# Optimization experiments

Hardware: AMD Instinct MI355X
Metric: run time of the kernel (lower is better)

The kernel has to match this reference:

```python
import jax, jax.numpy as jnp
import numpy as np

B, N, C = 2, 1024, 512
H = 8
HD = C // H  # 64
SCALE = HD ** -0.5


def setup_inputs() -> dict:
    key = jax.random.key(0)
    ks = jax.random.split(key, 10)
    q = jax.random.normal(ks[0], (B, N, C), jnp.float32)
    k = jax.random.normal(ks[1], (B, N, C), jnp.float32)
    v = jax.random.normal(ks[2], (B, N, C), jnp.float32)
    rel_pos_bias = jax.random.normal(ks[3], (B, N, N, HD), jnp.float32)
    # float padding mask: 0 for valid tokens, large negative for padded ones
    key_padding_mask = jnp.where(
        jax.random.uniform(ks[4], (B, N)) > 0.1, 0.0, -1e4
    ).astype(jnp.float32)
    Wq = jax.random.normal(ks[5], (C, C), jnp.float32) * 0.02
    Wk = jax.random.normal(ks[6], (C, C), jnp.float32) * 0.02
    Wv = jax.random.normal(ks[7], (C, C), jnp.float32) * 0.02
    Wp = jax.random.normal(ks[8], (C, C), jnp.float32) * 0.02
    bp = jnp.zeros((C,), jnp.float32)
    return {"q": q, "k": k, "v": v, "rel_pos_bias": rel_pos_bias,
            "key_padding_mask": key_padding_mask,
            "Wq": Wq, "Wk": Wk, "Wv": Wv, "Wp": Wp, "bp": bp}


def reference(q, k, v, rel_pos_bias, key_padding_mask, Wq, Wk, Wv, Wp, bp):
    # QKV projections, split heads: [B,H,N,HD]
    qh = (q @ Wq).reshape(B, N, H, HD).transpose(0, 2, 1, 3) * SCALE
    kh = (k @ Wk).reshape(B, N, H, HD).transpose(0, 2, 1, 3)
    vh = (v @ Wv).reshape(B, N, H, HD).transpose(0, 2, 1, 3)
    # scores + relative-bias injection into logits
    attn = jnp.einsum('bhid,bhjd->bhij', qh, kh)
    attn = attn + jnp.einsum('bhic,bijc->bhij', qh, rel_pos_bias)
    # float padding mask -> pairwise additive bias
    m = key_padding_mask
    pair = jnp.minimum(m[:, None, :], m[:, :, None])
    pair = jnp.where(jnp.maximum(m[:, None, :], m[:, :, None]) < 0, 0.0, pair)
    attn = attn + pair[:, None, :, :]
    attn = jax.nn.softmax(attn, axis=-1)
    # weighted values, with relative-bias injection into output
    x = jnp.einsum('bhij,bhjd->bihd', attn, vh)
    x = x + jnp.einsum('bhij,bijc->bihc', attn, rel_pos_bias)
    x = x.reshape(B, N, H * HD)
    return x @ Wp + bp
```

## Files before the change

kernel.cpp:

```cpp
#include <hip/hip_runtime.h>
#include <hip/hip_bf16.h>


typedef __attribute__((ext_vector_type(8))) short short8;
typedef __attribute__((ext_vector_type(4))) short short4v;
typedef __attribute__((ext_vector_type(4))) float f32x4;

#if defined(__has_builtin)
#  if __has_builtin(__builtin_amdgcn_mfma_f32_16x16x16bf16_1k)
#    define HAVE_MFMA16 1
#  endif
#endif
#ifndef HAVE_MFMA16
#  define HAVE_MFMA16 0
#endif

__device__ __forceinline__ unsigned short f2b(float f) {
    union { float f; unsigned u; } v; v.f = f;
    unsigned r = (v.u + 0x7FFF + ((v.u >> 16) & 1)) >> 16;
    return (unsigned short)r;
}

__device__ __forceinline__ unsigned cvt_pk(float a, float b) {
    unsigned r;
    asm("v_cvt_pk_bf16_f32 %0, %1, %2" : "=v"(r) : "v"(a), "v"(b));
    return r;
}

#define LGKM0_BAR()                                            \
    do {                                                       \
        asm volatile("s_waitcnt lgkmcnt(0)" ::: "memory");     \
        __builtin_amdgcn_s_barrier();                          \
        asm volatile("" ::: "memory");                         \
    } while (0)

__global__ __launch_bounds__(256) void wprep(
    const float* __restrict__ W0, const float* __restrict__ W1,
    const float* __restrict__ W2, unsigned short* __restrict__ WT)
{
    const int z = blockIdx.z;
    const float* W = (z == 0) ? W0 : ((z == 1) ? W1 : W2);
    unsigned short* T = WT + (size_t)z * 262144;
    __shared__ float Ts[64][65];
    const int t = threadIdx.x;
    const int k0 = blockIdx.x * 64, n0 = blockIdx.y * 64;
    const int kr = t >> 2, nc = (t & 3) * 16;
    #pragma unroll
    for (int q = 0; q < 4; ++q) {
        float4 v = *reinterpret_cast<const float4*>(
            W + (size_t)(k0 + kr) * 512 + n0 + nc + q * 4);
        Ts[kr][nc + q * 4 + 0] = v.x; Ts[kr][nc + q * 4 + 1] = v.y;
        Ts[kr][nc + q * 4 + 2] = v.z; Ts[kr][nc + q * 4 + 3] = v.w;
    }
    __syncthreads();
    const int nl = t >> 2, kc = (t & 3) * 16;
    unsigned short tmp[16];
    #pragma unroll
    for (int e = 0; e < 16; ++e) tmp[e] = f2b(Ts[kc + e][nl]);
    unsigned short* dst = T + (size_t)(n0 + nl) * 512 + k0 + kc;
    *reinterpret_cast<short8*>(dst)     = *reinterpret_cast<short8*>(&tmp[0]);
    *reinterpret_cast<short8*>(dst + 8) = *reinterpret_cast<short8*>(&tmp[8]);
}

__global__ __launch_bounds__(256) void proj_mfma(
    const float* __restrict__ qg, const float* __restrict__ kg,
    const float* __restrict__ vg, const unsigned short* __restrict__ WT,
    unsigned short* __restrict__ qhb, unsigned short* __restrict__ khb,
    unsigned short* __restrict__ vtb)
{
    const int z = blockIdx.z;
    const float* X = (z == 0) ? qg : ((z == 1) ? kg : vg);
    const unsigned short* WTz = WT + (size_t)z * 262144;
    const float scale = (z == 0) ? 0.125f : 1.0f;

    __shared__ unsigned short As[64][72];
    const int t = threadIdx.x, w = t >> 6, l = t & 63;
    const int l16 = l & 15, lg = l >> 4;
    const int m0 = blockIdx.x * 64, n0 = blockIdx.y * 64;
    const int ra = t >> 2, kc = (t & 3) * 16;

    f32x4 acc[4];
    #pragma unroll
    for (int cs = 0; cs < 4; ++cs) acc[cs] = 0.0f;

    for (int k0 = 0; k0 < 512; k0 += 64) {
        float4 va[4];
        #pragma unroll
        for (int qq = 0; qq < 4; ++qq)
            va[qq] = *reinterpret_cast<const float4*>(
                X + (size_t)(m0 + ra) * 512 + k0 + kc + qq * 4);
        uint4 pk0, pk1;
        pk0.x = cvt_pk(va[0].x, va[0].y); pk0.y = cvt_pk(va[0].z, va[0].w);
        pk0.z = cvt_pk(va[1].x, va[1].y); pk0.w = cvt_pk(va[1].z, va[1].w);
        pk1.x = cvt_pk(va[2].x, va[2].y); pk1.y = cvt_pk(va[2].z, va[2].w);
        pk1.z = cvt_pk(va[3].x, va[3].y); pk1.w = cvt_pk(va[3].z, va[3].w);
        __syncthreads();
        *reinterpret_cast<uint4*>(&As[ra][kc])     = pk0;
        *reinterpret_cast<uint4*>(&As[ra][kc + 8]) = pk1;
        __syncthreads();
        #pragma unroll
        for (int kk = 0; kk < 2; ++kk) {
            short8 a = *reinterpret_cast<const short8*>(
                &As[w * 16 + l16][kk * 32 + 8 * lg]);
            #pragma unroll
            for (int cs = 0; cs < 4; ++cs) {
                short8 b = *reinterpret_cast<const short8*>(
                    WTz + (size_t)(n0 + cs * 16 + l16) * 512 + k0 + kk * 32 + 8 * lg);
                acc[cs] = __builtin_amdgcn_mfma_f32_16x16x32_bf16(a, b, acc[cs], 0, 0, 0);
            }
        }
    }

    const int h = blockIdx.y;
    if (z < 2) {
        unsigned short* Y = (z == 0) ? qhb : khb;
        #pragma unroll
        for (int cs = 0; cs < 4; ++cs)
            #pragma unroll
            for (int r = 0; r < 4; ++r) {
                int m = m0 + w * 16 + lg * 4 + r;
                int bb = m >> 10, nn = m & 1023;
                Y[(((size_t)((bb * 8 + h) * 1024 + nn)) << 6) + cs * 16 + l16] =
                    f2b(acc[cs][r] * scale);
            }
    } else {
        int mbase = m0 + w * 16 + lg * 4;
        int bb = mbase >> 10, nn = mbase & 1023;
        #pragma unroll
        for (int cs = 0; cs < 4; ++cs) {
            ushort4 o;
            o.x = f2b(acc[cs][0]); o.y = f2b(acc[cs][1]);
            o.z = f2b(acc[cs][2]); o.w = f2b(acc[cs][3]);
            *reinterpret_cast<ushort4*>(
                vtb + (((size_t)(bb * 8 + h) * 64 + cs * 16 + l16) << 10) + nn) = o;
        }
    }
}

template <int MODE>
__global__ __launch_bounds__(256) void gemm512(
    const float* __restrict__ X, const float* __restrict__ W,
    const float* __restrict__ bias, float* __restrict__ Yf,
    unsigned short* __restrict__ Ybf, float scale)
{
    __shared__ float As[32][68];
    __shared__ float Bs[32][68];
    const int t  = threadIdx.x;
    const int tx = t & 15, ty = t >> 4;
    const int m0 = blockIdx.x * 64;
    const int n0 = blockIdx.y * 64;

    float acc[4][4] = {};

    for (int k0 = 0; k0 < 512; k0 += 32) {
        #pragma unroll
        for (int l = 0; l < 2; l++) {
            int qi = t + l * 256;
            int r = qi >> 3, q = qi & 7;
            float4 av = *reinterpret_cast<const float4*>(
                X + (size_t)(m0 + r) * 512 + k0 + q * 4);
            As[q * 4 + 0][r] = av.x; As[q * 4 + 1][r] = av.y;
            As[q * 4 + 2][r] = av.z; As[q * 4 + 3][r] = av.w;
        }
        #pragma unroll
        for (int l = 0; l < 2; l++) {
            int qi = t + l * 256;
            int kk = qi >> 4, q = qi & 15;
            *reinterpret_cast<float4*>(&Bs[kk][q * 4]) =
                *reinterpret_cast<const float4*>(
                    W + (size_t)(k0 + kk) * 512 + n0 + q * 4);
        }
        __syncthreads();
        #pragma unroll
        for (int kk = 0; kk < 32; kk++) {
            float4 a4 = *reinterpret_cast<const float4*>(&As[kk][ty * 4]);
            float4 b4 = *reinterpret_cast<const float4*>(&Bs[kk][tx * 4]);
            float av[4] = {a4.x, a4.y, a4.z, a4.w};
            float bv[4] = {b4.x, b4.y, b4.z, b4.w};
            #pragma unroll
            for (int ii = 0; ii < 4; ii++)
                #pragma unroll
                for (int jj = 0; jj < 4; jj++)
                    acc[ii][jj] = fmaf(av[ii], bv[jj], acc[ii][jj]);
        }
        __syncthreads();
    }

    float4 bv = *reinterpret_cast<const float4*>(bias + n0 + tx * 4);
    #pragma unroll
    for (int ii = 0; ii < 4; ii++) {
        int m = m0 + ty * 4 + ii;
        float4 o;
        o.x = acc[ii][0] + bv.x; o.y = acc[ii][1] + bv.y;
        o.z = acc[ii][2] + bv.z; o.w = acc[ii][3] + bv.w;
        *reinterpret_cast<float4*>(Yf + (size_t)m * 512 + n0 + tx * 4) = o;
    }
    (void)Ybf; (void)scale;
}

__global__ __launch_bounds__(512, 2) void attn_mfma(
    const unsigned short* __restrict__ qhg, const unsigned short* __restrict__ khg,
    const unsigned short* __restrict__ vtg, const float* __restrict__ rpb,
    const float* __restrict__ mask, float* __restrict__ xpart,
    float* __restrict__ lsump)
{
    __shared__ unsigned short rpb_s[2][16][16][72];
    __shared__ unsigned short khs[8][16][72];
    __shared__ unsigned short vts[8][64][24];
    __shared__ unsigned short q1[8][16][72];
    __shared__ unsigned short P[8][16][40];
    __shared__ float S2s[16][8][17];
    __shared__ float mask_s[512];

    const int bid = blockIdx.x;
    const int js = bid & 1, it = (bid >> 1) & 63, b = bid >> 7;
    const int i0 = it * 16, jb = js * 512;
    const int t = threadIdx.x, w = t >> 6, l = t & 63;
    const int lg = l >> 4, l16 = l & 15;

    const int sj = (t >> 3) & 15, sc = (t & 7) * 8, sib = t >> 7;
    const int kh_h = t >> 6, kh_j = (t >> 2) & 15, kh_c = (t & 3) * 16;
    const int vt_h = t >> 6, vt_c = t & 63;

    const float* rpbb = rpb + ((size_t)(b * 1024 + i0) << 16);

#define RPB_ISSUE(PF, J0)                                                      \
    _Pragma("unroll")                                                          \
    for (int itr = 0; itr < 4; ++itr) {                                        \
        const float4* s_ = reinterpret_cast<const float4*>(                    \
            rpbb + ((size_t)(sib + 4 * itr) << 16) +                           \
            (size_t)((J0) + sj) * 64 + sc);                                    \
        PF[2 * itr] = s_[0]; PF[2 * itr + 1] = s_[1];                          \
    }

#define RPB_WRITE(PF, BUF)                                                     \
    _Pragma("unroll")                                                          \
    for (int itr = 0; itr < 4; ++itr) {                                        \
        float4 ua = PF[2 * itr], ub = PF[2 * itr + 1];                         \
        uint4 pk;                                                              \
        pk.x = cvt_pk(ua.x, ua.y); pk.y = cvt_pk(ua.z, ua.w);                  \
        pk.z = cvt_pk(ub.x, ub.y); pk.w = cvt_pk(ub.z, ub.w);                  \
        *reinterpret_cast<uint4*>(&rpb_s[BUF][sib + 4 * itr][sj][sc]) = pk;    \
    }

#define KH_ISSUE(KP, J0)                                                       \
    {                                                                          \
        const unsigned short* p_ = khg + ((size_t)(b * 8 + kh_h) << 16) +      \
            (size_t)((J0) + kh_j) * 64 + kh_c;                                 \
        KP[0] = *reinterpret_cast<const short8*>(p_);                          \
        KP[1] = *reinterpret_cast<const short8*>(p_ + 8);                      \
    }

#define KH_WRITE(KP)                                                           \
    {                                                                          \
        *reinterpret_cast<short8*>(&khs[kh_h][kh_j][kh_c])     = KP[0];        \
        *reinterpret_cast<short8*>(&khs[kh_h][kh_j][kh_c + 8]) = KP[1];        \
    }

#define VT_ISSUE(VP, J0)                                                       \
    {                                                                          \
        const unsigned short* p_ = vtg + ((size_t)(b * 8 + vt_h) << 16) +      \
            ((size_t)vt_c << 10) + (J0);                                       \
        VP[0] = *reinterpret_cast<const short8*>(p_);                          \
        VP[1] = *reinterpret_cast<const short8*>(p_ + 8);                      \
    }

#define VT_WRITE(VP)                                                           \
    {                                                                          \
        *reinterpret_cast<short8*>(&vts[vt_h][vt_c][0]) = VP[0];               \
        *reinterpret_cast<short8*>(&vts[vt_h][vt_c][8]) = VP[1];               \
    }

    {
        int h = t >> 6, i = (t >> 2) & 15, c = (t & 3) * 16;
        const short8* src = reinterpret_cast<const short8*>(
            qhg + (((size_t)(b * 8 + h) * 1024 + i0 + i) << 6) + c);
        *reinterpret_cast<short8*>(&q1[h][i][c])     = src[0];
        *reinterpret_cast<short8*>(&q1[h][i][c + 8]) = src[1];
    }
    if (t < 128) {
        *reinterpret_cast<float4*>(&mask_s[t * 4]) =
            *reinterpret_cast<const float4*>(&mask[b * 1024 + jb + t * 4]);
    }
    {
        unsigned short* P1 = &P[0][0][0];
        #pragma unroll
        for (int r = 0; r < 10; ++r) P1[t + 512 * r] = 0;
    }
    float mrow[4];
    #pragma unroll
    for (int r = 0; r < 4; r++) mrow[r] = mask[b * 1024 + i0 + lg * 4 + r];

    float4 pfA[8], pfB[8];
    short8 kpfA[2], kpfB[2], vpfA[2], vpfB[2];
    RPB_ISSUE(pfA, jb)
    KH_ISSUE(kpfA, jb)
    VT_ISSUE(vpfA, jb)

    LGKM0_BAR();

    short8 a1[2];
    a1[0] = *reinterpret_cast<const short8*>(&q1[w][l16][8 * lg]);
    a1[1] = *reinterpret_cast<const short8*>(&q1[w][l16][32 + 8 * lg]);
    short8 bq[2][2];
    #pragma unroll
    for (int il = 0; il < 2; ++il) {
        bq[il][0] = *reinterpret_cast<const short8*>(
            &q1[l16 & 7][2 * w + il][8 * lg]);
        bq[il][1] = *reinterpret_cast<const short8*>(
            &q1[l16 & 7][2 * w + il][32 + 8 * lg]);
    }

    const int jo = (lg < 2) ? 8 * lg : 0;
    const int ro = jo;
    (void)ro;

    f32x4 x1[4];
    #pragma unroll
    for (int cs = 0; cs < 4; cs++) x1[cs] = 0.0f;
    f32x4 x2[2][4];
    #pragma unroll
    for (int il = 0; il < 2; il++)
        #pragma unroll
        for (int cg = 0; cg < 4; cg++) x2[il][cg] = 0.0f;
    float lsum[4] = {0.f, 0.f, 0.f, 0.f};

#define ATTN_ITER(T, PFC, KPC, VPC, PFN, KPN, VPN)                             \
    {                                                                          \
        const int jt = (T);                                                    \
        const int cur = jt & 1;                                                \
        const int j0 = jb + jt * 16;                                           \
        if (jt < 31) {                                                         \
            RPB_ISSUE(PFN, j0 + 16)                                            \
            KH_ISSUE(KPN, j0 + 16)                                             \
            VT_ISSUE(VPN, j0 + 16)                                             \
        }                                                                      \
        RPB_WRITE(PFC, cur)                                                    \
        KH_WRITE(KPC)                                                          \
        VT_WRITE(VPC)                                                          \
        LGKM0_BAR();                                                           \
        f32x4 C1; C1 = 0.0f;                                                   \
        {                                                                      \
            short8 kb0 = *reinterpret_cast<const short8*>(&khs[w][l16][8 * lg]); \
            short8 kb1 = *reinterpret_cast<const short8*>(&khs[w][l16][32 + 8 * lg]); \
            C1 = __builtin_amdgcn_mfma_f32_16x16x32_bf16(a1[0], kb0, C1, 0, 0, 0); \
            C1 = __builtin_amdgcn_mfma_f32_16x16x32_bf16(a1[1], kb1, C1, 0, 0, 0); \
        }                                                                      \
        _Pragma("unroll")                                                      \
        for (int il = 0; il < 2; ++il) {                                       \
            int i = 2 * w + il;                                                \
            f32x4 D2; D2 = 0.0f;                                               \
            _Pragma("unroll")                                                  \
            for (int ch = 0; ch < 2; ++ch) {                                   \
                short8 ar = *reinterpret_cast<const short8*>(                  \
                    &rpb_s[cur][i][l16][ch * 32 + 8 * lg]);                    \
                D2 = __builtin_amdgcn_mfma_f32_16x16x32_bf16(ar, bq[il][ch], D2, 0, 0, 0); \
            }                                                                  \
            if (l16 < 8) {                                                     \
                _Pragma("unroll")                                              \
                for (int r = 0; r < 4; ++r)                                    \
                    S2s[i][l16][4 * lg + r] = D2[r];                           \
            }                                                                  \
        }                                                                      \
        LGKM0_BAR();                                                           \
        {                                                                      \
            float mj = mask_s[jt * 16 + l16];                                  \
            _Pragma("unroll")                                                  \
            for (int r = 0; r < 4; ++r) {                                      \
                int ir = lg * 4 + r;                                           \
                float mi = mrow[r];                                            \
                float pm = (fmaxf(mi, mj) < 0.f) ? 0.f : fminf(mi, mj);        \
                float s = C1[r] + S2s[ir][w][l16] + pm;                        \
                float p = __expf(s);                                           \
                lsum[r] += p;                                                  \
                P[w][ir][l16] = f2b(p);                                        \
            }                                                                  \
        }                                                                      \
        LGKM0_BAR();                                                           \
        X1X2_BODY(cur)                                                         \
        LGKM0_BAR();                                                           \
    }

#if HAVE_MFMA16
#define X1X2_BODY(CUR)                                                         \
    {                                                                          \
        short4v pa = *reinterpret_cast<const short4v*>(&P[w][l16][4 * lg]);    \
        _Pragma("unroll")                                                      \
        for (int cs = 0; cs < 4; ++cs) {                                       \
            short4v vb = *reinterpret_cast<const short4v*>(                    \
                &vts[w][cs * 16 + l16][4 * lg]);                               \
            x1[cs] = __builtin_amdgcn_mfma_f32_16x16x16bf16_1k(pa, vb, x1[cs], 0, 0, 0); \
        }                                                                      \
    }                                                                          \
    _Pragma("unroll")                                                          \
    for (int il = 0; il < 2; ++il) {                                           \
        int i = 2 * w + il;                                                    \
        short4v pa2 = *reinterpret_cast<const short4v*>(&P[l16 & 7][i][4 * lg]); \
        _Pragma("unroll")                                                      \
        for (int cg = 0; cg < 4; ++cg) {                                       \
            short4v bb;                                                        \
            _Pragma("unroll")                                                  \
            for (int e = 0; e < 4; ++e)                                        \
                bb[e] = (short)rpb_s[CUR][i][4 * lg + e][cg * 16 + l16];       \
            x2[il][cg] = __builtin_amdgcn_mfma_f32_16x16x16bf16_1k(pa2, bb, x2[il][cg], 0, 0, 0); \
        }                                                                      \
    }
#else
#define X1X2_BODY(CUR)                                                         \
    {                                                                          \
        short8 pa = *reinterpret_cast<const short8*>(&P[w][l16][8 * lg]);      \
        _Pragma("unroll")                                                      \
        for (int cs = 0; cs < 4; ++cs) {                                       \
            short8 vb = *reinterpret_cast<const short8*>(                      \
                &vts[w][cs * 16 + l16][jo]);                                   \
            x1[cs] = __builtin_amdgcn_mfma_f32_16x16x32_bf16(pa, vb, x1[cs], 0, 0, 0); \
        }                                                                      \
    }                                                                          \
    _Pragma("unroll")                                                          \
    for (int il = 0; il < 2; ++il) {                                           \
        int i = 2 * w + il;                                                    \
        short8 pa2 = *reinterpret_cast<const short8*>(&P[l16 & 7][i][8 * lg]); \
        _Pragma("unroll")                                                      \
        for (int cg = 0; cg < 4; ++cg) {                                       \
            short8 bb;                                                         \
            _Pragma("unroll")                                                  \
            for (int e = 0; e < 8; ++e)                                        \
                bb[e] = (short)rpb_s[CUR][i][ro + e][cg * 16 + l16];           \
            x2[il][cg] = __builtin_amdgcn_mfma_f32_16x16x32_bf16(pa2, bb, x2[il][cg], 0, 0, 0); \
        }                                                                      \
    }
#endif

    for (int th = 0; th < 16; ++th) {
        ATTN_ITER(2 * th,     pfA, kpfA, vpfA, pfB, kpfB, vpfB)
        ATTN_ITER(2 * th + 1, pfB, kpfB, vpfB, pfA, kpfA, vpfA)
    }

    #pragma unroll
    for (int r = 0; r < 4; ++r) {
        float v = lsum[r];
        v += __shfl_xor(v, 1, 64); v += __shfl_xor(v, 2, 64);
        v += __shfl_xor(v, 4, 64); v += __shfl_xor(v, 8, 64);
        lsum[r] = v;
    }

    __syncthreads();
    float* x2s = reinterpret_cast<float*>(&rpb_s[0][0][0][0]);
    if (lg < 2) {
        #pragma unroll
        for (int il = 0; il < 2; ++il)
            #pragma unroll
            for (int cg = 0; cg < 4; ++cg)
                #pragma unroll
                for (int r = 0; r < 4; ++r)
                    x2s[((2 * w + il) * 8 + 4 * lg + r) * 64 + cg * 16 + l16] =
                        x2[il][cg][r];
    }
    __syncthreads();

    #pragma unroll
    for (int cs = 0; cs < 4; ++cs)
        #pragma unroll
        for (int r = 0; r < 4; ++r) {
            int ir = lg * 4 + r;
            float val = x1[cs][r] + x2s[(ir * 8 + w) * 64 + cs * 16 + l16];
            xpart[((size_t)js << 20) + ((size_t)(b * 1024 + i0 + ir)) * 512
                  + w * 64 + cs * 16 + l16] = val;
        }
    if (l16 == 0) {
        #pragma unroll
        for (int r = 0; r < 4; ++r)
            lsump[((size_t)js << 14) + (b * 8 + w) * 1024 + i0 + lg * 4 + r] = lsum[r];
    }
#undef ATTN_ITER
#undef X1X2_BODY
#undef RPB_ISSUE
#undef RPB_WRITE
#undef KH_ISSUE
#undef KH_WRITE
#undef VT_ISSUE
#undef VT_WRITE
}

__global__ __launch_bounds__(256) void combine(
    const float* __restrict__ xpart, const float* __restrict__ lsump,
    float* __restrict__ xb)
{
    int idx4 = blockIdx.x * 256 + threadIdx.x;
    size_t base = (size_t)idx4 * 4;
    int row = (int)(base >> 9), col = (int)(base & 511);
    int bb = row >> 10, n = row & 1023, h = col >> 6;
    float ax = 0.f, ay = 0.f, az = 0.f, aw = 0.f, ls = 0.f;
    #pragma unroll
    for (int js = 0; js < 2; ++js) {
        float4 v = *reinterpret_cast<const float4*>(xpart + ((size_t)js << 20) + base);
        ax += v.x; ay += v.y; az += v.z; aw += v.w;
        ls += lsump[(js << 14) + (bb * 8 + h) * 1024 + n];
    }
    float inv = 1.f / ls;
    float4 o; o.x = ax * inv; o.y = ay * inv; o.z = az * inv; o.w = aw * inv;
    *reinterpret_cast<float4*>(xb + base) = o;
}

extern "C" void kernel_launch(void* const* d_in, const int* in_sizes, int n_in,
                              void* d_out, int out_size, void* d_ws, size_t ws_size,
                              hipStream_t stream)
{
    (void)in_sizes; (void)n_in; (void)out_size; (void)ws_size;
    const float* q    = (const float*)d_in[0];
    const float* k    = (const float*)d_in[1];
    const float* v    = (const float*)d_in[2];
    const float* rpb  = (const float*)d_in[3];
    const float* mask = (const float*)d_in[4];
    const float* Wq   = (const float*)d_in[5];
    const float* Wk   = (const float*)d_in[6];
    const float* Wv   = (const float*)d_in[7];
    const float* Wp   = (const float*)d_in[8];
    const float* bp   = (const float*)d_in[9];
    float* out = (float*)d_out;

    unsigned short* qhb = (unsigned short*)d_ws;
    unsigned short* khb = qhb + 1048576;
    unsigned short* vtb = khb + 1048576;
    float* xpart = (float*)(vtb + 1048576);
    float* lsump = xpart + 2097152;
    float* xb    = lsump + 32768;
    unsigned short* wT = (unsigned short*)(xb + 1048576);

    wprep<<<dim3(8, 8, 3), 256, 0, stream>>>(Wq, Wk, Wv, wT);

    proj_mfma<<<dim3(32, 8, 3), 256, 0, stream>>>(q, k, v, wT, qhb, khb, vtb);

    attn_mfma<<<256, 512, 0, stream>>>(qhb, khb, vtb, rpb, mask, xpart, lsump);

    combine<<<1024, 256, 0, stream>>>(xpart, lsump, xb);

    gemm512<1><<<dim3(32, 8, 1), 256, 0, stream>>>(xb, Wp, bp, out, nullptr, 1.0f);
}
```

Before: 189.2 us.

## Fuse split-combine into output projection and run it on split-bf16 MFMA

Removes the separate combine kernel and the FP32 scalar output-projection GEMM. A new out_mfma kernel sums the two partial outputs, normalizes them by the summed lsum on load, and splits both activations and Wp into bf16 hi/lo pairs. It then does three MFMA products to keep near-fp32 accuracy. wprep now also converts Wp into hi/lo transposed bf16 copies, which adds some prep work and MFMA volume in exchange for tensor-core throughput and one fewer launch and intermediate buffer.

```diff
diff --git a/kernel.cpp b/kernel.cpp
--- a/kernel.cpp
+++ b/kernel.cpp
@@ -20,6 +20,10 @@
     unsigned r = (v.u + 0x7FFF + ((v.u >> 16) & 1)) >> 16;
     return (unsigned short)r;
 }
+__device__ __forceinline__ float b2f(unsigned short h) {
+    union { unsigned u; float f; } v; v.u = ((unsigned)h) << 16;
+    return v.f;
+}
 
 __device__ __forceinline__ unsigned cvt_pk(float a, float b) {
     unsigned r;
@@ -36,11 +40,11 @@
 
 __global__ __launch_bounds__(256) void wprep(
     const float* __restrict__ W0, const float* __restrict__ W1,
-    const float* __restrict__ W2, unsigned short* __restrict__ WT)
+    const float* __restrict__ W2, const float* __restrict__ W3,
+    unsigned short* __restrict__ WT)
 {
     const int z = blockIdx.z;
-    const float* W = (z == 0) ? W0 : ((z == 1) ? W1 : W2);
-    unsigned short* T = WT + (size_t)z * 262144;
+    const float* W = (z == 0) ? W0 : ((z == 1) ? W1 : ((z == 2) ? W2 : W3));
     __shared__ float Ts[64][65];
     const int t = threadIdx.x;
     const int k0 = blockIdx.x * 64, n0 = blockIdx.y * 64;
@@ -54,12 +58,31 @@
     }
     __syncthreads();
     const int nl = t >> 2, kc = (t & 3) * 16;
-    unsigned short tmp[16];
-    #pragma unroll
-    for (int e = 0; e < 16; ++e) tmp[e] = f2b(Ts[kc + e][nl]);
-    unsigned short* dst = T + (size_t)(n0 + nl) * 512 + k0 + kc;
-    *reinterpret_cast<short8*>(dst)     = *reinterpret_cast<short8*>(&tmp[0]);
-    *reinterpret_cast<short8*>(dst + 8) = *reinterpret_cast<short8*>(&tmp[8]);
+    if (z < 3) {
+        unsigned short* T = WT + (size_t)z * 262144;
+        unsigned short tmp[16];
+        #pragma unroll
+        for (int e = 0; e < 16; ++e) tmp[e] = f2b(Ts[kc + e][nl]);
+        unsigned short* dst = T + (size_t)(n0 + nl) * 512 + k0 + kc;
+        *reinterpret_cast<short8*>(dst)     = *reinterpret_cast<short8*>(&tmp[0]);
+        *reinterpret_cast<short8*>(dst + 8) = *reinterpret_cast<short8*>(&tmp[8]);
+    } else {
+        unsigned short* Th = WT + (size_t)3 * 262144;
+        unsigned short* Tl = WT + (size_t)4 * 262144;
+        unsigned short hi[16], lo[16];
+        #pragma unroll
+        for (int e = 0; e < 16; ++e) {
+            float v = Ts[kc + e][nl];
+            hi[e] = f2b(v);
+            lo[e] = f2b(v - b2f(hi[e]));
+        }
+        unsigned short* dh = Th + (size_t)(n0 + nl) * 512 + k0 + kc;
+        unsigned short* dl = Tl + (size_t)(n0 + nl) * 512 + k0 + kc;
+        *reinterpret_cast<short8*>(dh)     = *reinterpret_cast<short8*>(&hi[0]);
+        *reinterpret_cast<short8*>(dh + 8) = *reinterpret_cast<short8*>(&hi[8]);
+        *reinterpret_cast<short8*>(dl)     = *reinterpret_cast<short8*>(&lo[0]);
+        *reinterpret_cast<short8*>(dl + 8) = *reinterpret_cast<short8*>(&lo[8]);
+    }
 }
 
 __global__ __launch_bounds__(256) void proj_mfma(
@@ -137,65 +160,77 @@
     }
 }
 
-template <int MODE>
-__global__ __launch_bounds__(256) void gemm512(
-    const float* __restrict__ X, const float* __restrict__ W,
-    const float* __restrict__ bias, float* __restrict__ Yf,
-    unsigned short* __restrict__ Ybf, float scale)
+__global__ __launch_bounds__(256) void out_mfma(
+    const float* __restrict__ xpart, const float* __restrict__ lsump,
+    const unsigned short* __restrict__ WT, const float* __restrict__ bp,
+    float* __restrict__ out)
 {
-    __shared__ float As[32][68];
-    __shared__ float Bs[32][68];
-    const int t  = threadIdx.x;
-    const int tx = t & 15, ty = t >> 4;
-    const int m0 = blockIdx.x * 64;
-    const int n0 = blockIdx.y * 64;
-
-    float acc[4][4] = {};
-
-    for (int k0 = 0; k0 < 512; k0 += 32) {
-        #pragma unroll
-        for (int l = 0; l < 2; l++) {
-            int qi = t + l * 256;
-            int r = qi >> 3, q = qi & 7;
-            float4 av = *reinterpret_cast<const float4*>(
-                X + (size_t)(m0 + r) * 512 + k0 + q * 4);
-            As[q * 4 + 0][r] = av.x; As[q * 4 + 1][r] = av.y;
-            As[q * 4 + 2][r] = av.z; As[q * 4 + 3][r] = av.w;
-        }
-        #pragma unroll
-        for (int l = 0; l < 2; l++) {
-            int qi = t + l * 256;
-            int kk = qi >> 4, q = qi & 15;
-            *reinterpret_cast<float4*>(&Bs[kk][q * 4]) =
-                *reinterpret_cast<const float4*>(
-                    W + (size_t)(k0 + kk) * 512 + n0 + q * 4);
+    const unsigned short* WPhi = WT + (size_t)3 * 262144;
+    const unsigned short* WPlo = WT + (size_t)4 * 262144;
+    __shared__ unsigned short Ah[64][72];
+    __shared__ unsigned short Al[64][72];
+    const int t = threadIdx.x, w = t >> 6, l = t & 63;
+    const int l16 = l & 15, lg = l >> 4;
+    const int m0 = blockIdx.x * 64, n0 = blockIdx.y * 64;
+    const int ra = t >> 2, kc = (t & 3) * 16;
+    const int mrow = m0 + ra, bb = mrow >> 10, nn = mrow & 1023;
+
+    f32x4 acc[4];
+    #pragma unroll
+    for (int cs = 0; cs < 4; ++cs) acc[cs] = 0.0f;
+
+    for (int k0 = 0; k0 < 512; k0 += 64) {
+        const int h = k0 >> 6;
+        float ls = lsump[(bb * 8 + h) * 1024 + nn]
+                 + lsump[16384 + (bb * 8 + h) * 1024 + nn];
+        float inv = 1.0f / ls;
+        unsigned short hi[16], lo[16];
+        #pragma unroll
+        for (int qq = 0; qq < 4; ++qq) {
+            size_t base = ((size_t)(bb * 1024 + nn)) * 512 + k0 + kc + qq * 4;
+            float4 v0 = *reinterpret_cast<const float4*>(xpart + base);
+            float4 v1 = *reinterpret_cast<const float4*>(xpart + (1u << 20) + base);
+            float e0 = (v0.x + v1.x) * inv, e1 = (v0.y + v1.y) * inv;
+            float e2 = (v0.z + v1.z) * inv, e3 = (v0.w + v1.w) * inv;
+            hi[qq * 4 + 0] = f2b(e0); lo[qq * 4 + 0] = f2b(e0 - b2f(hi[qq * 4 + 0]));
+            hi[qq * 4 + 1] = f2b(e1); lo[qq * 4 + 1] = f2b(e1 - b2f(hi[qq * 4 + 1]));
+            hi[qq * 4 + 2] = f2b(e2); lo[qq * 4 + 2] = f2b(e2 - b2f(hi[qq * 4 + 2]));
+            hi[qq * 4 + 3] = f2b(e3); lo[qq * 4 + 3] = f2b(e3 - b2f(hi[qq * 4 + 3]));
         }
         __syncthreads();
-        #pragma unroll
-        for (int kk = 0; kk < 32; kk++) {
-            float4 a4 = *reinterpret_cast<const float4*>(&As[kk][ty * 4]);
-            float4 b4 = *reinterpret_cast<const float4*>(&Bs[kk][tx * 4]);
-            float av[4] = {a4.x, a4.y, a4.z, a4.w};
-            float bv[4] = {b4.x, b4.y, b4.z, b4.w};
+        *reinterpret_cast<short8*>(&Ah[ra][kc])     = *reinterpret_cast<short8*>(&hi[0]);
+        *reinterpret_cast<short8*>(&Ah[ra][kc + 8]) = *reinterpret_cast<short8*>(&hi[8]);
+        *reinterpret_cast<short8*>(&Al[ra][kc])     = *reinterpret_cast<short8*>(&lo[0]);
+        *reinterpret_cast<short8*>(&Al[ra][kc + 8]) = *reinterpret_cast<short8*>(&lo[8]);
+        __syncthreads();
+        #pragma unroll
+        for (int kk = 0; kk < 2; ++kk) {
+            short8 ah = *reinterpret_cast<const short8*>(
+                &Ah[w * 16 + l16][kk * 32 + 8 * lg]);
+            short8 al = *reinterpret_cast<const short8*>(
+                &Al[w * 16 + l16][kk * 32 + 8 * lg]);
             #pragma unroll
-            for (int ii = 0; ii < 4; ii++)
-                #pragma unroll
-                for (int jj = 0; jj < 4; jj++)
-                    acc[ii][jj] = fmaf(av[ii], bv[jj], acc[ii][jj]);
-        }
-        __syncthreads();
-    }
-
-    float4 bv = *reinterpret_cast<const float4*>(bias + n0 + tx * 4);
-    #pragma unroll
-    for (int ii = 0; ii < 4; ii++) {
-        int m = m0 + ty * 4 + ii;
-        float4 o;
-        o.x = acc[ii][0] + bv.x; o.y = acc[ii][1] + bv.y;
-        o.z = acc[ii][2] + bv.z; o.w = acc[ii][3] + bv.w;
-        *reinterpret_cast<float4*>(Yf + (size_t)m * 512 + n0 + tx * 4) = o;
-    }
-    (void)Ybf; (void)scale;
+            for (int cs = 0; cs < 4; ++cs) {
+                size_t wb = (size_t)(n0 + cs * 16 + l16) * 512 + k0 + kk * 32 + 8 * lg;
+                short8 bh = *reinterpret_cast<const short8*>(WPhi + wb);
+                short8 bl = *reinterpret_cast<const short8*>(WPlo + wb);
+                acc[cs] = __builtin_amdgcn_mfma_f32_16x16x32_bf16(ah, bh, acc[cs], 0, 0, 0);
+                acc[cs] = __builtin_amdgcn_mfma_f32_16x16x32_bf16(ah, bl, acc[cs], 0, 0, 0);
+                acc[cs] = __builtin_amdgcn_mfma_f32_16x16x32_bf16(al, bh, acc[cs], 0, 0, 0);
+            }
+        }
+    }
+
+    #pragma unroll
+    for (int cs = 0; cs < 4; ++cs) {
+        int col = n0 + cs * 16 + l16;
+        float bv = bp[col];
+        #pragma unroll
+        for (int r = 0; r < 4; ++r) {
+            int row = m0 + w * 16 + lg * 4 + r;
+            out[(size_t)row * 512 + col] = acc[cs][r] + bv;
+        }
+    }
 }
 
 __global__ __launch_bounds__(512, 2) void attn_mfma(
@@ -480,26 +515,6 @@
 #undef KH_WRITE
 #undef VT_ISSUE
 #undef VT_WRITE
-}
-
-__global__ __launch_bounds__(256) void combine(
-    const float* __restrict__ xpart, const float* __restrict__ lsump,
-    float* __restrict__ xb)
-{
-    int idx4 = blockIdx.x * 256 + threadIdx.x;
-    size_t base = (size_t)idx4 * 4;
-    int row = (int)(base >> 9), col = (int)(base & 511);
-    int bb = row >> 10, n = row & 1023, h = col >> 6;
-    float ax = 0.f, ay = 0.f, az = 0.f, aw = 0.f, ls = 0.f;
-    #pragma unroll
-    for (int js = 0; js < 2; ++js) {
-        float4 v = *reinterpret_cast<const float4*>(xpart + ((size_t)js << 20) + base);
-        ax += v.x; ay += v.y; az += v.z; aw += v.w;
-        ls += lsump[(js << 14) + (bb * 8 + h) * 1024 + n];
-    }
-    float inv = 1.f / ls;
-    float4 o; o.x = ax * inv; o.y = ay * inv; o.z = az * inv; o.w = aw * inv;
-    *reinterpret_cast<float4*>(xb + base) = o;
 }
 
 extern "C" void kernel_launch(void* const* d_in, const int* in_sizes, int n_in,
@@ -524,16 +539,13 @@
     unsigned short* vtb = khb + 1048576;
     float* xpart = (float*)(vtb + 1048576);
     float* lsump = xpart + 2097152;
-    float* xb    = lsump + 32768;
-    unsigned short* wT = (unsigned short*)(xb + 1048576);
-
-    wprep<<<dim3(8, 8, 3), 256, 0, stream>>>(Wq, Wk, Wv, wT);
+    unsigned short* wT = (unsigned short*)(lsump + 32768);
+
+    wprep<<<dim3(8, 8, 4), 256, 0, stream>>>(Wq, Wk, Wv, Wp, wT);
 
     proj_mfma<<<dim3(32, 8, 3), 256, 0, stream>>>(q, k, v, wT, qhb, khb, vtb);
 
     attn_mfma<<<256, 512, 0, stream>>>(qhb, khb, vtb, rpb, mask, xpart, lsump);
 
-    combine<<<1024, 256, 0, stream>>>(xpart, lsump, xb);
-
-    gemm512<1><<<dim3(32, 8, 1), 256, 0, stream>>>(xb, Wp, bp, out, nullptr, 1.0f);
-}
+    out_mfma<<<dim3(32, 8), 256, 0, stream>>>(xpart, lsump, wT, bp, out);
+}
```

New measurement: 185.1 us. -2.2%, faster.
